# Kernel tuning notes

Hardware: AMD Instinct MI355X
Metric: run time of the kernel (lower is better)

## Reference

```python
import jax, jax.numpy as jnp
import numpy as np
import math

D = 1280      # embed_dim ('650M')
H = 20        # n_head
DH = D // H   # d_hidden = 64
DFF = 4 * D   # r_ff = 4
LN_EPS = 1e-5


def layer_norm(x, gamma, beta):
    mu = jnp.mean(x, axis=-1, keepdims=True)
    var = jnp.var(x, axis=-1, keepdims=True)
    return (x - mu) * jax.lax.rsqrt(var + LN_EPS) * gamma + beta


def setup_inputs() -> dict:
    key = jax.random.key(0)
    ks = jax.random.split(key, 16)
    B, L = 2, 2048
    x = jax.random.normal(ks[0], (B, L, D), dtype=jnp.float32)
    y = jax.random.normal(ks[1], (B, L, D), dtype=jnp.float32)  # dm_embeds (unused by module)
    s_qkv = 1.0 / math.sqrt(D)
    Wq = jax.random.uniform(ks[2], (D, D), jnp.float32, -s_qkv, s_qkv)
    Wk = jax.random.uniform(ks[3], (D, D), jnp.float32, -s_qkv, s_qkv)
    Wv = jax.random.uniform(ks[4], (D, D), jnp.float32, -s_qkv, s_qkv)
    Wo = jax.random.uniform(ks[5], (D, D), jnp.float32, -s_qkv, s_qkv)
    bo = jnp.zeros((D,), jnp.float32)
    W1 = jax.random.normal(ks[6], (D, DFF), jnp.float32) * math.sqrt(2.0 / D)  # kaiming
    b1 = jnp.zeros((DFF,), jnp.float32)
    W2 = jax.random.uniform(ks[7], (DFF, D), jnp.float32, -1.0 / math.sqrt(DFF), 1.0 / math.sqrt(DFF))
    b2 = jnp.zeros((D,), jnp.float32)
    g1 = jnp.ones((D,), jnp.float32); be1 = jnp.zeros((D,), jnp.float32)
    g2 = jnp.ones((D,), jnp.float32); be2 = jnp.zeros((D,), jnp.float32)
    return dict(x=x, y=y, Wq=Wq, Wk=Wk, Wv=Wv, Wo=Wo, bo=bo,
                W1=W1, b1=b1, W2=W2, b2=b2, g1=g1, be1=be1, g2=g2, be2=be2)


def reference(x, y, Wq, Wk, Wv, Wo, bo, W1, b1, W2, b2, g1, be1, g2, be2):
    B, L, _ = x.shape
    scaling = 1.0 / math.sqrt(DH)
    # --- pre-norm self-attention ---
    xn = layer_norm(x, g1, be1)
    q = (xn @ Wq).reshape(B, L, H, DH) * scaling
    k = (xn @ Wk).reshape(B, L, H, DH)
    v = (xn @ Wv).reshape(B, L, H, DH)
    scores = jnp.einsum('bqhd,bkhd->bhqk', q, k)
    attn = jax.nn.softmax(scores, axis=-1)
    o = jnp.einsum('bhqk,bkhd->bqhd', attn, v).reshape(B, L, D)
    x = x + (o @ Wo + bo)
    # --- pre-norm FFN ---
    xn = layer_norm(x, g2, be2)
    h = jax.nn.relu(xn @ W1 + b1)
    x = x + (h @ W2 + b2)
    return x
```

## Files before the change

kernel.cpp:

```cpp
#include <hip/hip_runtime.h>

typedef short bf16x8 __attribute__((ext_vector_type(8)));
typedef short bf16x4 __attribute__((ext_vector_type(4)));
typedef float f32x4 __attribute__((ext_vector_type(4)));
typedef unsigned short u16;

#define GL16(g, l) __builtin_amdgcn_global_load_lds( \
    (const __attribute__((address_space(1))) void*)(g), \
    (__attribute__((address_space(3))) void*)(l), 16, 0, 0)

__device__ __forceinline__ u16 f2bf(float f) {
  union { float f; unsigned u; } v; v.f = f;
  return (u16)((v.u + 0x7fffu + ((v.u >> 16) & 1u)) >> 16);
}

__device__ __forceinline__ float exp2_(float x) {
#if __has_builtin(__builtin_amdgcn_exp2f)
  return __builtin_amdgcn_exp2f(x);
#else
  return __expf(x * 0.69314718056f);
#endif
}

__device__ __forceinline__ unsigned cvtpk(float a, float b) {
  unsigned r;
  asm("v_cvt_pk_bf16_f32 %0, %1, %2" : "=v"(r) : "v"(a), "v"(b));
  return r;
}

__global__ __launch_bounds__(256) void ln_kernel(
    const float* __restrict__ x, const float* __restrict__ g,
    const float* __restrict__ b, u16* __restrict__ out) {
  const int row = blockIdx.x, tid = threadIdx.x;
  const float4* xr = (const float4*)(x + (size_t)row * 1280);
  float4 v1 = xr[tid];
  float4 v2 = make_float4(0.f, 0.f, 0.f, 0.f);
  if (tid < 64) v2 = xr[256 + tid];
  float s = v1.x + v1.y + v1.z + v1.w + v2.x + v2.y + v2.z + v2.w;
  float q = v1.x * v1.x + v1.y * v1.y + v1.z * v1.z + v1.w * v1.w +
            v2.x * v2.x + v2.y * v2.y + v2.z * v2.z + v2.w * v2.w;
#pragma unroll
  for (int off = 32; off >= 1; off >>= 1) {
    s += __shfl_xor(s, off);
    q += __shfl_xor(q, off);
  }
  __shared__ float sm[8];
  if ((tid & 63) == 0) { sm[tid >> 6] = s; sm[4 + (tid >> 6)] = q; }
  __syncthreads();
  s = sm[0] + sm[1] + sm[2] + sm[3];
  q = sm[4] + sm[5] + sm[6] + sm[7];
  const float mean = s * (1.0f / 1280.0f);
  const float rstd = rsqrtf(q * (1.0f / 1280.0f) - mean * mean + 1e-5f);
  const float4* gr = (const float4*)g;
  const float4* br = (const float4*)b;
  u16* orow = out + (size_t)row * 1280;
  {
    float4 gg = gr[tid], bb = br[tid];
    ushort4 o;
    o.x = f2bf((v1.x - mean) * rstd * gg.x + bb.x);
    o.y = f2bf((v1.y - mean) * rstd * gg.y + bb.y);
    o.z = f2bf((v1.z - mean) * rstd * gg.z + bb.z);
    o.w = f2bf((v1.w - mean) * rstd * gg.w + bb.w);
    *(ushort4*)&orow[tid * 4] = o;
  }
  if (tid < 64) {
    float4 gg = gr[256 + tid], bb = br[256 + tid];
    ushort4 o;
    o.x = f2bf((v2.x - mean) * rstd * gg.x + bb.x);
    o.y = f2bf((v2.y - mean) * rstd * gg.y + bb.y);
    o.z = f2bf((v2.z - mean) * rstd * gg.z + bb.z);
    o.w = f2bf((v2.w - mean) * rstd * gg.w + bb.w);
    *(ushort4*)&orow[(256 + tid) * 4] = o;
  }
}

__global__ __launch_bounds__(256) void tconv_kernel(
    const float* __restrict__ src, u16* __restrict__ dst,
    int rows, int cols, float scale) {
  __shared__ float t[64][33];
  const int tid = threadIdx.x;
  const size_t c0 = (size_t)blockIdx.x * 64, r0 = (size_t)blockIdx.y * 32;
  const int ty = tid >> 4, col4 = tid & 15;
#pragma unroll
  for (int i = 0; i < 2; ++i) {
    const int row = ty + i * 16;
    float4 v = *(const float4*)&src[(r0 + row) * cols + c0 + col4 * 4];
    t[col4 * 4 + 0][row] = v.x;
    t[col4 * 4 + 1][row] = v.y;
    t[col4 * 4 + 2][row] = v.z;
    t[col4 * 4 + 3][row] = v.w;
  }
  __syncthreads();
  const int c = tid >> 2, rb = (tid & 3) * 8;
  ushort4 o1, o2;
  o1.x = f2bf(t[c][rb + 0] * scale); o1.y = f2bf(t[c][rb + 1] * scale);
  o1.z = f2bf(t[c][rb + 2] * scale); o1.w = f2bf(t[c][rb + 3] * scale);
  o2.x = f2bf(t[c][rb + 4] * scale); o2.y = f2bf(t[c][rb + 5] * scale);
  o2.z = f2bf(t[c][rb + 6] * scale); o2.w = f2bf(t[c][rb + 7] * scale);
  u16* d = &dst[(c0 + c) * rows + r0 + rb];
  *(ushort4*)d = o1;
  *(ushort4*)(d + 4) = o2;
}

__global__ __launch_bounds__(256) void tconv3_kernel(
    const float* __restrict__ s0, const float* __restrict__ s1,
    const float* __restrict__ s2, u16* __restrict__ dst, float scale0) {
  __shared__ float t[64][33];
  const int tid = threadIdx.x, z = blockIdx.z;
  const float* src = (z == 0) ? s0 : ((z == 1) ? s1 : s2);
  const float scale = (z == 0) ? scale0 : 1.0f;
  u16* d0 = dst + (size_t)z * 1280 * 1280;
  const size_t c0 = (size_t)blockIdx.x * 64, r0 = (size_t)blockIdx.y * 32;
  const int ty = tid >> 4, col4 = tid & 15;
#pragma unroll
  for (int i = 0; i < 2; ++i) {
    const int row = ty + i * 16;
    float4 v = *(const float4*)&src[(r0 + row) * 1280 + c0 + col4 * 4];
    t[col4 * 4 + 0][row] = v.x;
    t[col4 * 4 + 1][row] = v.y;
    t[col4 * 4 + 2][row] = v.z;
    t[col4 * 4 + 3][row] = v.w;
  }
  __syncthreads();
  const int c = tid >> 2, rb = (tid & 3) * 8;
  ushort4 o1, o2;
  o1.x = f2bf(t[c][rb + 0] * scale); o1.y = f2bf(t[c][rb + 1] * scale);
  o1.z = f2bf(t[c][rb + 2] * scale); o1.w = f2bf(t[c][rb + 3] * scale);
  o2.x = f2bf(t[c][rb + 4] * scale); o2.y = f2bf(t[c][rb + 5] * scale);
  o2.z = f2bf(t[c][rb + 6] * scale); o2.w = f2bf(t[c][rb + 7] * scale);
  u16* d = &d0[(c0 + c) * 1280 + r0 + rb];
  *(ushort4*)d = o1;
  *(ushort4*)(d + 4) = o2;
}

__global__ __launch_bounds__(256) void vtrans_kernel(const u16* __restrict__ qkv,
                                                     u16* __restrict__ vt) {
  __shared__ u16 t[64][65];
  const int tx = threadIdx.x & 63, ty = threadIdx.x >> 6;
  const int t0 = blockIdx.x * 64, bh = blockIdx.y, b = bh / 20, h = bh % 20;
  const u16* src = qkv + (size_t)b * 2048 * 3840 + 2560 + h * 64;
  for (int i = ty; i < 64; i += 4) t[i][tx] = src[(size_t)(t0 + i) * 3840 + tx];
  __syncthreads();
  u16* dst = vt + (size_t)bh * 64 * 2048 + t0;
  for (int i = ty; i < 64; i += 4) dst[(size_t)i * 2048 + tx] = t[tx][i];
}

__global__ __launch_bounds__(256) void initadd_kernel(
    const float* __restrict__ src, const float* __restrict__ bias,
    float* __restrict__ out) {
  const size_t i = (size_t)blockIdx.x * 256 + threadIdx.x;
  float4 v = ((const float4*)src)[i];
  float4 b = ((const float4*)bias)[i % 320];
  v.x += b.x; v.y += b.y; v.z += b.z; v.w += b.w;
  ((float4*)out)[i] = v;
}

template <int EPI>
__device__ __forceinline__ void gemm_body(
    const u16* __restrict__ A, const u16* __restrict__ BT,
    const float* __restrict__ bias, void* __restrict__ out,
    int M, int N, int K, int kSteps) {
  __shared__ __attribute__((aligned(16))) u16 Als[3][128 * 32];
  __shared__ __attribute__((aligned(16))) u16 Bls[3][128 * 32];
  const int tid = threadIdx.x;
  const int w = tid >> 6, lane = tid & 63;
  const int lo = lane & 15, hi = lane >> 4;
  const int wm = w >> 1, wn = w & 1;
  const int gx = gridDim.x, gxy = gx * gridDim.y;
  const int nwg = gxy * gridDim.z;
  int s = blockIdx.x + gx * blockIdx.y + gxy * blockIdx.z;
  s = (s & 7) * (nwg >> 3) + (s >> 3);
  const int bz = s / gxy; s -= bz * gxy;
  const int by = s / gx;  const int bx = s - by * gx;
  const size_t m0 = (size_t)by * 128, n0 = (size_t)bx * 128;
  const int kt0 = bz * kSteps;
  f32x4 acc[4][4] = {};
  const int srow = w * 32 + (lane >> 2);
  const int scol = ((lane & 3) ^ ((lane >> 3) & 3)) * 8;
  const int rsw = (lo >> 1) & 3;
#define STAGE(buf, kt)                                                        \
  do {                                                                        \
    const size_t kb = (size_t)(kt) * 32 + scol;                               \
    GL16(&A[(m0 + srow) * K + kb],       &Als[buf][(w * 2 + 0) * 512]);       \
    GL16(&A[(m0 + srow + 16) * K + kb],  &Als[buf][(w * 2 + 1) * 512]);       \
    GL16(&BT[(n0 + srow) * K + kb],      &Bls[buf][(w * 2 + 0) * 512]);       \
    GL16(&BT[(n0 + srow + 16) * K + kb], &Bls[buf][(w * 2 + 1) * 512]);       \
  } while (0)
  STAGE(0, kt0 + 0);
  STAGE(1, kt0 + 1);
  int cur = 0;
  for (int t = 0; t < kSteps; ++t) {
    if (t + 1 < kSteps) asm volatile("s_waitcnt vmcnt(4)" ::: "memory");
    else                asm volatile("s_waitcnt vmcnt(0)" ::: "memory");
    __builtin_amdgcn_s_barrier();
    __builtin_amdgcn_sched_barrier(0);
    const int nxt = (cur == 0) ? 2 : cur - 1;
    if (t + 2 < kSteps) STAGE(nxt, kt0 + t + 2);
    bf16x8 af[4], bfr[4];
#pragma unroll
    for (int mi = 0; mi < 4; ++mi)
      af[mi] = *(const bf16x8*)&Als[cur][(wm * 64 + mi * 16 + lo) * 32 + ((hi ^ rsw) * 8)];
#pragma unroll
    for (int ni = 0; ni < 4; ++ni)
      bfr[ni] = *(const bf16x8*)&Bls[cur][(wn * 64 + ni * 16 + lo) * 32 + ((hi ^ rsw) * 8)];
#pragma unroll
    for (int mi = 0; mi < 4; ++mi)
#pragma unroll
      for (int ni = 0; ni < 4; ++ni)
        acc[mi][ni] = __builtin_amdgcn_mfma_f32_16x16x32_bf16(
            af[mi], bfr[ni], acc[mi][ni], 0, 0, 0);
    cur = (cur == 2) ? 0 : cur + 1;
  }
#undef STAGE
#pragma unroll
  for (int ni = 0; ni < 4; ++ni) {
    const size_t col = n0 + wn * 64 + ni * 16 + lo;
    const float bv = (EPI == 1) ? bias[col] : 0.0f;
#pragma unroll
    for (int mi = 0; mi < 4; ++mi) {
      const size_t rb = m0 + wm * 64 + mi * 16 + hi * 4;
#pragma unroll
      for (int r = 0; r < 4; ++r) {
        const size_t idx = (rb + r) * N + col;
        float v = acc[mi][ni][r];
        if (EPI == 0) {
          ((u16*)out)[idx] = f2bf(v);
        } else if (EPI == 1) {
          v += bv;
          v = fmaxf(v, 0.0f);
          ((u16*)out)[idx] = f2bf(v);
        } else {
          atomicAdd(&((float*)out)[idx], v);
        }
      }
    }
  }
}

__global__ __launch_bounds__(256, 3) void gemm_qkv(
    const u16* __restrict__ A, const u16* __restrict__ BT,
    void* __restrict__ out, int M, int N, int K, int kSteps) {
  gemm_body<0>(A, BT, nullptr, out, M, N, K, kSteps);
}
__global__ __launch_bounds__(256, 3) void gemm_oproj(
    const u16* __restrict__ A, const u16* __restrict__ BT,
    void* __restrict__ out, int M, int N, int K, int kSteps) {
  gemm_body<3>(A, BT, nullptr, out, M, N, K, kSteps);
}
__global__ __launch_bounds__(256, 3) void gemm_ffn1(
    const u16* __restrict__ A, const u16* __restrict__ BT,
    const float* __restrict__ bias, void* __restrict__ out,
    int M, int N, int K, int kSteps) {
  gemm_body<1>(A, BT, bias, out, M, N, K, kSteps);
}
__global__ __launch_bounds__(256, 3) void gemm_ffn2(
    const u16* __restrict__ A, const u16* __restrict__ BT,
    void* __restrict__ out, int M, int N, int K, int kSteps) {
  gemm_body<3>(A, BT, nullptr, out, M, N, K, kSteps);
}

__global__ __launch_bounds__(512) void attn_kernel(
    const u16* __restrict__ qkv, const u16* __restrict__ vt,
    u16* __restrict__ aout) {
  __shared__ __attribute__((aligned(16))) u16 Klds[64 * 64];
  __shared__ __attribute__((aligned(16))) u16 Vlds[64 * 64];
  __shared__ __attribute__((aligned(16))) u16 Plds[8][16][72];
  const int tid = threadIdx.x;
  const int w = tid >> 6, lane = tid & 63;
  const int lo = lane & 15, hi = lane >> 4;
  const int bh = blockIdx.x, qt = blockIdx.y;
  const int b = bh / 20, h = bh % 20;
  const size_t qrow = (size_t)b * 2048 + qt * 128 + w * 16 + lo;
  bf16x8 qf[2];
  qf[0] = *(const bf16x8*)&qkv[qrow * 3840 + h * 64 + hi * 8];
  qf[1] = *(const bf16x8*)&qkv[qrow * 3840 + h * 64 + 32 + hi * 8];
  float m_i = -1e30f, l_i = 0.0f;
  f32x4 accO[4] = {};
  const int srow = lane >> 3;
  const int scol = ((lane & 7) ^ srow) * 8;
  const u16* kbase = qkv + (size_t)b * 2048 * 3840 + 1280 + h * 64;
  const u16* vbase = vt + (size_t)bh * 64 * 2048;
  for (int kt = 0; kt < 32; ++kt) {
    {
      const int row = w * 8 + srow;
      GL16(kbase + (size_t)(kt * 64 + row) * 3840 + scol, &Klds[w * 512]);
      GL16(vbase + (size_t)row * 2048 + kt * 64 + scol, &Vlds[w * 512]);
    }
    __syncthreads();
    f32x4 s4[4] = {};
    __builtin_amdgcn_s_setprio(1);
#pragma unroll
    for (int st = 0; st < 4; ++st) {
      const int row = st * 16 + lo;
      const int sw = (row & 7) << 3;
#pragma unroll
      for (int ks = 0; ks < 2; ++ks) {
        bf16x8 a = *(const bf16x8*)&Klds[row * 64 + ((ks * 32 + hi * 8) ^ sw)];
        s4[st] = __builtin_amdgcn_mfma_f32_16x16x32_bf16(a, qf[ks], s4[st], 0, 0, 0);
      }
    }
    __builtin_amdgcn_s_setprio(0);
    float tm = fmaxf(fmaxf(fmaxf(s4[0][0], s4[0][1]), fmaxf(s4[0][2], s4[0][3])),
                     fmaxf(fmaxf(s4[1][0], s4[1][1]), fmaxf(s4[1][2], s4[1][3])));
    tm = fmaxf(tm, fmaxf(fmaxf(fmaxf(s4[2][0], s4[2][1]), fmaxf(s4[2][2], s4[2][3])),
                         fmaxf(fmaxf(s4[3][0], s4[3][1]), fmaxf(s4[3][2], s4[3][3]))));
    tm = fmaxf(tm, __shfl_xor(tm, 16));
    tm = fmaxf(tm, __shfl_xor(tm, 32));
    if (!__all(tm <= m_i + 8.0f)) {
      const float mnew = fmaxf(m_i, tm);
      const float corr = exp2_(m_i - mnew);
      m_i = mnew;
      l_i *= corr;
      float cr[4];
#pragma unroll
      for (int r = 0; r < 4; ++r) cr[r] = __shfl(corr, hi * 4 + r);
#pragma unroll
      for (int d = 0; d < 4; ++d)
#pragma unroll
        for (int r = 0; r < 4; ++r) accO[d][r] *= cr[r];
    }
#pragma unroll
    for (int st = 0; st < 4; ++st)
#pragma unroll
      for (int r = 0; r < 4; ++r) {
        const float p = exp2_(s4[st][r] - m_i);
        s4[st][r] = p;
        l_i += p;
      }
#pragma unroll
    for (int st = 0; st < 4; ++st) {
      uint2 pk;
      pk.x = cvtpk(s4[st][0], s4[st][1]);
      pk.y = cvtpk(s4[st][2], s4[st][3]);
      *(uint2*)&Plds[w][lo][st * 16 + hi * 4] = pk;
    }
    asm volatile("s_waitcnt lgkmcnt(0)" ::: "memory");
    __builtin_amdgcn_sched_barrier(0);
    __builtin_amdgcn_s_setprio(1);
#pragma unroll
    for (int ks = 0; ks < 2; ++ks) {
      bf16x8 pa = *(const bf16x8*)&Plds[w][lo][ks * 32 + hi * 8];
#pragma unroll
      for (int d = 0; d < 4; ++d) {
        const int row = d * 16 + lo;
        bf16x8 vb = *(const bf16x8*)
            &Vlds[row * 64 + ((ks * 32 + hi * 8) ^ ((row & 7) << 3))];
        accO[d] = __builtin_amdgcn_mfma_f32_16x16x32_bf16(pa, vb, accO[d], 0, 0, 0);
      }
    }
    __builtin_amdgcn_s_setprio(0);
    __syncthreads();
  }
  l_i += __shfl_xor(l_i, 16);
  l_i += __shfl_xor(l_i, 32);
  float linv[4];
#pragma unroll
  for (int r = 0; r < 4; ++r) linv[r] = 1.0f / __shfl(l_i, hi * 4 + r);
  const size_t orow0 = (size_t)b * 2048 + qt * 128 + w * 16 + hi * 4;
#pragma unroll
  for (int d = 0; d < 4; ++d)
#pragma unroll
    for (int r = 0; r < 4; ++r)
      aout[(orow0 + r) * 1280 + h * 64 + d * 16 + lo] =
          f2bf(accO[d][r] * linv[r]);
}

extern "C" void kernel_launch(void* const* d_in, const int* in_sizes, int n_in,
                              void* d_out, int out_size, void* d_ws, size_t ws_size,
                              hipStream_t stream) {
  const float* x   = (const float*)d_in[0];
  const float* Wq  = (const float*)d_in[2];
  const float* Wk  = (const float*)d_in[3];
  const float* Wv  = (const float*)d_in[4];
  const float* Wo  = (const float*)d_in[5];
  const float* bo  = (const float*)d_in[6];
  const float* W1  = (const float*)d_in[7];
  const float* b1  = (const float*)d_in[8];
  const float* W2  = (const float*)d_in[9];
  const float* b2  = (const float*)d_in[10];
  const float* g1  = (const float*)d_in[11];
  const float* be1 = (const float*)d_in[12];
  const float* g2  = (const float*)d_in[13];
  const float* be2 = (const float*)d_in[14];

  u16* xn   = (u16*)d_ws;
  u16* Wqkv = xn + (size_t)4096 * 1280;
  u16* WoT  = Wqkv + (size_t)3840 * 1280;
  u16* W1T  = WoT + (size_t)1280 * 1280;
  u16* W2T  = W1T + (size_t)5120 * 1280;
  u16* aOut = W2T + (size_t)1280 * 5120;
  float* x1 = (float*)(aOut + (size_t)4096 * 1280);
  u16* qkvb = (u16*)(x1 + (size_t)4096 * 1280);
  u16* vtb  = qkvb + (size_t)4096 * 3840;
  u16* hbuf = qkvb;

  const float qscale = 0.125f * 1.4426950408889634f;
  ln_kernel<<<4096, 256, 0, stream>>>(x, g1, be1, xn);
  tconv3_kernel<<<dim3(20, 40, 3), 256, 0, stream>>>(Wq, Wk, Wv, Wqkv, qscale);
  tconv_kernel<<<dim3(20, 40), 256, 0, stream>>>(Wo, WoT, 1280, 1280, 1.0f);
  tconv_kernel<<<dim3(80, 40), 256, 0, stream>>>(W1, W1T, 1280, 5120, 1.0f);
  tconv_kernel<<<dim3(20, 160), 256, 0, stream>>>(W2, W2T, 5120, 1280, 1.0f);
  gemm_qkv<<<dim3(30, 32), 256, 0, stream>>>(xn, Wqkv, qkvb, 4096, 3840, 1280, 40);
  vtrans_kernel<<<dim3(32, 40), 256, 0, stream>>>(qkvb, vtb);
  attn_kernel<<<dim3(40, 16), 512, 0, stream>>>(qkvb, vtb, aOut);
  initadd_kernel<<<5120, 256, 0, stream>>>(x, bo, x1);
  gemm_oproj<<<dim3(10, 32, 2), 256, 0, stream>>>(aOut, WoT, x1, 4096, 1280, 1280, 20);
  ln_kernel<<<4096, 256, 0, stream>>>(x1, g2, be2, xn);
  gemm_ffn1<<<dim3(40, 32), 256, 0, stream>>>(xn, W1T, b1, hbuf, 4096, 5120, 1280, 40);
  initadd_kernel<<<5120, 256, 0, stream>>>(x1, b2, (float*)d_out);
  gemm_ffn2<<<dim3(10, 32, 2), 256, 0, stream>>>(hbuf, W2T, d_out, 4096, 1280, 5120, 80);
  (void)in_sizes; (void)n_in; (void)out_size; (void)ws_size;
}
```

Measured before the change: 407.8 us.

## Replace QKV GEMM with 256x256-tile 8-wave pipelined kernel

Adds a new GEMM body that uses 256x256 output tiles and 512 threads. Each K step is split into four quadrant phases, so the global-to-LDS prefetch for the next step overlaps with MFMA work on the current one, with priority boosts and XCD-aware block remapping. It replaces the previous 128-tile QKV GEMM launch. The aim is more operand reuse per LDS load and better latency hiding. The trade-offs are 128 KB of LDS per block and only 240 workgroups, which may leave some CUs underused.

```diff
diff --git a/kernel.cpp b/kernel.cpp
--- a/kernel.cpp
+++ b/kernel.cpp
@@ -237,11 +237,6 @@
   }
 }
 
-__global__ __launch_bounds__(256, 3) void gemm_qkv(
-    const u16* __restrict__ A, const u16* __restrict__ BT,
-    void* __restrict__ out, int M, int N, int K, int kSteps) {
-  gemm_body<0>(A, BT, nullptr, out, M, N, K, kSteps);
-}
 __global__ __launch_bounds__(256, 3) void gemm_oproj(
     const u16* __restrict__ A, const u16* __restrict__ BT,
     void* __restrict__ out, int M, int N, int K, int kSteps) {
@@ -257,6 +252,167 @@
     const u16* __restrict__ A, const u16* __restrict__ BT,
     void* __restrict__ out, int M, int N, int K, int kSteps) {
   gemm_body<3>(A, BT, nullptr, out, M, N, K, kSteps);
+}
+
+template <int EPI>
+__device__ __forceinline__ void gemm8v2_body(
+    const u16* __restrict__ A, const u16* __restrict__ BT,
+    const float* __restrict__ bias, void* __restrict__ out,
+    int M, int N, int K, int nt) {
+  __shared__ __attribute__((aligned(16))) u16 Als[2][2][128 * 64];
+  __shared__ __attribute__((aligned(16))) u16 Bls[2][2][128 * 64];
+  const int tid = threadIdx.x;
+  const int w = tid >> 6, lane = tid & 63;
+  const int lo = lane & 15, hi = lane >> 4;
+  const int wm = w >> 2, wn = w & 3;
+  const int gx = gridDim.x, gxy = gx * gridDim.y;
+  const int nwg = gxy * gridDim.z;
+  int s = blockIdx.x + gx * blockIdx.y + gxy * blockIdx.z;
+  s = (s & 7) * (nwg >> 3) + (s >> 3);
+  const int bz = s / gxy; s -= bz * gxy;
+  const int by = s / gx;  const int bx = s - by * gx;
+  const size_t m0 = (size_t)by * 256, n0 = (size_t)bx * 256;
+  const int kt0 = bz * nt;
+  f32x4 acc[8][4] = {};
+  const int srowo = lane >> 3;
+  const int gcol = ((lane & 7) ^ (lane >> 3)) * 8;
+  const int rsw = lo & 7;
+#define STG(dstbuf, srcp, rbase, kt)                                          \
+  do {                                                                        \
+    const size_t kb = (size_t)(kt) * 64 + gcol;                               \
+    GL16(&srcp[(rbase + w * 16 + srowo) * K + kb], &dstbuf[(w * 16) * 64]);   \
+    GL16(&srcp[(rbase + w * 16 + 8 + srowo) * K + kb],                        \
+         &dstbuf[(w * 16 + 8) * 64]);                                         \
+  } while (0)
+#define BAR()   __builtin_amdgcn_s_barrier()
+#define SB0()   __builtin_amdgcn_sched_barrier(0)
+#define LGKM0() asm volatile("s_waitcnt lgkmcnt(0)" ::: "memory")
+#define VM6()   asm volatile("s_waitcnt vmcnt(6)" ::: "memory")
+#define VM0()   asm volatile("s_waitcnt vmcnt(0)" ::: "memory")
+  STG(Als[0][0], A,  m0,       kt0 + 0);
+  STG(Bls[0][0], BT, n0,       kt0 + 0);
+  STG(Bls[1][0], BT, n0 + 128, kt0 + 0);
+  STG(Als[1][0], A,  m0 + 128, kt0 + 0);
+  for (int t = 0; t < nt; ++t) {
+    const int sl = t & 1, sn = sl ^ 1;
+    const bool pf = (t + 1 < nt);
+    bf16x8 a0[4][2], a1[4][2], b0[2][2], b1[2][2];
+    if (pf) { STG(Als[0][sn], A, m0, kt0 + t + 1); SB0(); VM6(); }
+    else    { VM0(); }
+    BAR(); SB0();
+#pragma unroll
+    for (int mi = 0; mi < 4; ++mi)
+#pragma unroll
+      for (int ks = 0; ks < 2; ++ks)
+        a0[mi][ks] = *(const bf16x8*)&Als[0][sl][(wm * 64 + mi * 16 + lo) * 64 +
+                                                (((ks * 4 + hi) ^ rsw) * 8)];
+#pragma unroll
+    for (int ni = 0; ni < 2; ++ni)
+#pragma unroll
+      for (int ks = 0; ks < 2; ++ks)
+        b0[ni][ks] = *(const bf16x8*)&Bls[0][sl][(wn * 32 + ni * 16 + lo) * 64 +
+                                                (((ks * 4 + hi) ^ rsw) * 8)];
+    LGKM0(); SB0();
+    __builtin_amdgcn_s_setprio(1);
+#pragma unroll
+    for (int mi = 0; mi < 4; ++mi)
+#pragma unroll
+      for (int ni = 0; ni < 2; ++ni)
+#pragma unroll
+        for (int ks = 0; ks < 2; ++ks)
+          acc[mi][ni] = __builtin_amdgcn_mfma_f32_16x16x32_bf16(
+              a0[mi][ks], b0[ni][ks], acc[mi][ni], 0, 0, 0);
+    __builtin_amdgcn_s_setprio(0);
+    if (pf) { STG(Bls[0][sn], BT, n0, kt0 + t + 1); SB0(); VM6(); }
+    else    { VM0(); }
+    BAR(); SB0();
+#pragma unroll
+    for (int ni = 0; ni < 2; ++ni)
+#pragma unroll
+      for (int ks = 0; ks < 2; ++ks)
+        b1[ni][ks] = *(const bf16x8*)&Bls[1][sl][(wn * 32 + ni * 16 + lo) * 64 +
+                                                (((ks * 4 + hi) ^ rsw) * 8)];
+    LGKM0(); SB0();
+    __builtin_amdgcn_s_setprio(1);
+#pragma unroll
+    for (int mi = 0; mi < 4; ++mi)
+#pragma unroll
+      for (int ni = 0; ni < 2; ++ni)
+#pragma unroll
+        for (int ks = 0; ks < 2; ++ks)
+          acc[mi][ni + 2] = __builtin_amdgcn_mfma_f32_16x16x32_bf16(
+              a0[mi][ks], b1[ni][ks], acc[mi][ni + 2], 0, 0, 0);
+    __builtin_amdgcn_s_setprio(0);
+    if (pf) { STG(Bls[1][sn], BT, n0 + 128, kt0 + t + 1); SB0(); VM6(); }
+    else    { VM0(); }
+    BAR(); SB0();
+#pragma unroll
+    for (int mi = 0; mi < 4; ++mi)
+#pragma unroll
+      for (int ks = 0; ks < 2; ++ks)
+        a1[mi][ks] = *(const bf16x8*)&Als[1][sl][(wm * 64 + mi * 16 + lo) * 64 +
+                                                (((ks * 4 + hi) ^ rsw) * 8)];
+    LGKM0(); SB0();
+    __builtin_amdgcn_s_setprio(1);
+#pragma unroll
+    for (int mi = 0; mi < 4; ++mi)
+#pragma unroll
+      for (int ni = 0; ni < 2; ++ni)
+#pragma unroll
+        for (int ks = 0; ks < 2; ++ks)
+          acc[mi + 4][ni] = __builtin_amdgcn_mfma_f32_16x16x32_bf16(
+              a1[mi][ks], b0[ni][ks], acc[mi + 4][ni], 0, 0, 0);
+    __builtin_amdgcn_s_setprio(0);
+    if (pf) STG(Als[1][sn], A, m0 + 128, kt0 + t + 1);
+    SB0();
+    __builtin_amdgcn_s_setprio(1);
+#pragma unroll
+    for (int mi = 0; mi < 4; ++mi)
+#pragma unroll
+      for (int ni = 0; ni < 2; ++ni)
+#pragma unroll
+        for (int ks = 0; ks < 2; ++ks)
+          acc[mi + 4][ni + 2] = __builtin_amdgcn_mfma_f32_16x16x32_bf16(
+              a1[mi][ks], b1[ni][ks], acc[mi + 4][ni + 2], 0, 0, 0);
+    __builtin_amdgcn_s_setprio(0);
+  }
+#undef STG
+#undef BAR
+#undef SB0
+#undef LGKM0
+#undef VM6
+#undef VM0
+#pragma unroll
+  for (int ni = 0; ni < 4; ++ni) {
+    const int ncol = (ni < 2) ? (wn * 32 + ni * 16) : (128 + wn * 32 + (ni - 2) * 16);
+    const size_t col = n0 + ncol + lo;
+    const float bv = (EPI == 1) ? bias[col] : 0.0f;
+#pragma unroll
+    for (int mi = 0; mi < 8; ++mi) {
+      const int mrow = (mi < 4) ? (wm * 64 + mi * 16) : (128 + wm * 64 + (mi - 4) * 16);
+      const size_t rb = m0 + mrow + hi * 4;
+#pragma unroll
+      for (int r = 0; r < 4; ++r) {
+        const size_t idx = (rb + r) * N + col;
+        float v = acc[mi][ni][r];
+        if (EPI == 0) {
+          ((u16*)out)[idx] = f2bf(v);
+        } else if (EPI == 1) {
+          v += bv;
+          v = fmaxf(v, 0.0f);
+          ((u16*)out)[idx] = f2bf(v);
+        } else {
+          atomicAdd(&((float*)out)[idx], v);
+        }
+      }
+    }
+  }
+}
+
+__global__ __launch_bounds__(512, 2) void gemm_qkv8(
+    const u16* __restrict__ A, const u16* __restrict__ BT,
+    void* __restrict__ out, int M, int N, int K, int nt) {
+  gemm8v2_body<0>(A, BT, nullptr, out, M, N, K, nt);
 }
 
 __global__ __launch_bounds__(512) void attn_kernel(
@@ -400,7 +556,7 @@
   tconv_kernel<<<dim3(20, 40), 256, 0, stream>>>(Wo, WoT, 1280, 1280, 1.0f);
   tconv_kernel<<<dim3(80, 40), 256, 0, stream>>>(W1, W1T, 1280, 5120, 1.0f);
   tconv_kernel<<<dim3(20, 160), 256, 0, stream>>>(W2, W2T, 5120, 1280, 1.0f);
-  gemm_qkv<<<dim3(30, 32), 256, 0, stream>>>(xn, Wqkv, qkvb, 4096, 3840, 1280, 40);
+  gemm_qkv8<<<dim3(15, 16), 512, 0, stream>>>(xn, Wqkv, qkvb, 4096, 3840, 1280, 20);
   vtrans_kernel<<<dim3(32, 40), 256, 0, stream>>>(qkvb, vtb);
   attn_kernel<<<dim3(40, 16), 512, 0, stream>>>(qkvb, vtb, aOut);
   initadd_kernel<<<5120, 256, 0, stream>>>(x, bo, x1);
```

New measurement: 385.8 us. 1.06x faster.
